# Kernel optimization log

Hardware: AMD Instinct MI355X
Metric: run time of the kernel (lower is better)

## Reference

```python
import jax, jax.numpy as jnp
import numpy as np

N, S, K, DIN, DOUT = 100000, 50000, 16, 256, 256


def setup_inputs() -> dict:
    key = jax.random.key(0)
    k1, k2, k3, k4 = jax.random.split(key, 4)
    word_vectors = jax.random.normal(k1, (N, DIN), dtype=jnp.float32)
    src_idx = jnp.arange(S, dtype=jnp.int64)  # unique source nodes
    neighs_idx = jax.random.randint(k2, (S, K), 0, N).astype(jnp.int64)
    src_mask = jax.random.uniform(k3, (S, K), dtype=jnp.float32)
    W = jax.random.normal(k4, (DOUT, DIN), dtype=jnp.float32) / np.sqrt(DIN)
    b = jnp.zeros((DOUT,), dtype=jnp.float32)
    return {"word_vectors": word_vectors, "src_idx": src_idx,
            "neighs_idx": neighs_idx, "src_mask": src_mask, "W": W, "b": b}


def reference(word_vectors, src_idx, neighs_idx, src_mask, W, b):
    # Linear projection: [N, DIN] @ [DIN, DOUT] + b -> [N, DOUT]
    supports = word_vectors @ W.T + b
    src_feats = supports[src_idx]          # [S, D]
    neigh_feats = supports[neighs_idx]     # [S, K, D]
    # masked neighbor aggregation ([S,1,K] x [S,K,D]) + residual
    outputs = jnp.einsum('sk,skd->sd', src_mask, neigh_feats) + src_feats
    # LeakyReLU(negative_slope=0.2)
    outputs = jnp.where(outputs >= 0, outputs, 0.2 * outputs)
    # scatter-add back into supports (src_idx unique -> matches torch in-place +=)
    supports = supports.at[src_idx].add(outputs)
    return supports
```

## Files before the change

kernel.cpp:

```cpp
#include <hip/hip_runtime.h>
#include <hip/hip_bf16.h>

#define DIN  256
#define DOUT 256
#define KNEI 16

typedef __attribute__((ext_vector_type(4))) float f32x4;
typedef __attribute__((ext_vector_type(8))) short bf16x8;
typedef __attribute__((ext_vector_type(4))) short bf16x4;

__device__ __forceinline__ short f2bf(float f) {
    unsigned int u;
    __builtin_memcpy(&u, &f, 4);
    unsigned int r = (u + 0x7fffu + ((u >> 16) & 1u)) >> 16;
    return (short)r;
}

__device__ __forceinline__ float bf2f(short s) {
    unsigned int u = ((unsigned int)(unsigned short)s) << 16;
    float f;
    __builtin_memcpy(&f, &u, 4);
    return f;
}

__global__ __launch_bounds__(256) void pack_w_kernel(
        const float* __restrict__ W, short* __restrict__ Wp) {
    int gid  = blockIdx.x * 256 + threadIdx.x;
    int lane = gid & 63;
    int frag = gid >> 6;
    int kb   = frag & 7;
    int cb   = frag >> 3;
    int col  = cb * 16 + (lane & 15);
    int k0   = kb * 32 + (lane >> 4) * 8;
    const float* src = W + (size_t)col * DIN + k0;
    bf16x8 v;
#pragma unroll
    for (int j = 0; j < 8; ++j) v[j] = f2bf(src[j]);
    *((bf16x8*)Wp + (size_t)frag * 64 + lane) = v;
}

__global__ __launch_bounds__(256) void gemm_kernel(
        const float* __restrict__ A, const short* __restrict__ Wp,
        const float* __restrict__ bias, float* __restrict__ out,
        short* __restrict__ out_bf, int M) {
    const int tid  = threadIdx.x;
    const int wid  = tid >> 6;
    const int lane = tid & 63;
    const int row0 = (blockIdx.x * 4 + wid) * 16;
    if (row0 >= M) return;

    const int r = row0 + (lane & 15);
    const int g = lane >> 4;

    const float* arow = A + (size_t)r * DIN + g * 8;
    f32x4 araw[16];
#pragma unroll
    for (int kb = 0; kb < 8; ++kb) {
        araw[2 * kb]     = *(const f32x4*)(arow + kb * 32);
        araw[2 * kb + 1] = *(const f32x4*)(arow + kb * 32 + 4);
    }
    bf16x8 afrag[8];
#pragma unroll
    for (int kb = 0; kb < 8; ++kb) {
#pragma unroll
        for (int j = 0; j < 4; ++j) {
            afrag[kb][j]     = f2bf(araw[2 * kb][j]);
            afrag[kb][4 + j] = f2bf(araw[2 * kb + 1][j]);
        }
    }

    f32x4 acc[16];
#pragma unroll
    for (int cb = 0; cb < 16; ++cb) acc[cb] = f32x4{0.f, 0.f, 0.f, 0.f};

    const bf16x8* wp = (const bf16x8*)Wp;
#pragma unroll
    for (int kb = 0; kb < 8; ++kb) {
#pragma unroll
        for (int cb = 0; cb < 16; ++cb) {
            bf16x8 w = wp[(size_t)(cb * 8 + kb) * 64 + lane];
            acc[cb] = __builtin_amdgcn_mfma_f32_16x16x32_bf16(
                w, afrag[kb], acc[cb], 0, 0, 0);
        }
    }

    float* orow = out    + (size_t)r * DOUT;
    short* brow = out_bf + (size_t)r * DOUT;
#pragma unroll
    for (int cb = 0; cb < 16; ++cb) {
        int c0 = cb * 16 + g * 4;
        f32x4 bv = *(const f32x4*)(bias + c0);
        f32x4 v  = acc[cb] + bv;
        __builtin_nontemporal_store(v, (f32x4*)(orow + c0));
        bf16x4 h;
#pragma unroll
        for (int j = 0; j < 4; ++j) h[j] = f2bf(v[j]);
        *(bf16x4*)(brow + c0) = h;
    }
}

__global__ __launch_bounds__(256) void aggregate_fused_kernel(
        const short* __restrict__ sup_bf, const int* __restrict__ src_idx,
        const int* __restrict__ neighs, const float* __restrict__ mask,
        float* __restrict__ out, int S) {
    int s = blockIdx.x * 4 + (threadIdx.x >> 6);
    if (s >= S) return;
    s = __builtin_amdgcn_readfirstlane(s);
    const int lane = threadIdx.x & 63;
    const int c4   = lane * 4;

    f32x4 acc = {0.f, 0.f, 0.f, 0.f};
#pragma unroll
    for (int k = 0; k < KNEI; ++k) {
        int   idx = neighs[(size_t)s * KNEI + k];
        float m   = mask[(size_t)s * KNEI + k];
        bf16x4 v = *(const bf16x4*)(sup_bf + (size_t)idx * DOUT + c4);
#pragma unroll
        for (int j = 0; j < 4; ++j) acc[j] += m * bf2f(v[j]);
    }

    int srow = src_idx[s];
    bf16x4 svh = *(const bf16x4*)(sup_bf + (size_t)srow * DOUT + c4);
    f32x4 res;
#pragma unroll
    for (int j = 0; j < 4; ++j) {
        float sv = bf2f(svh[j]);
        float o  = acc[j] + sv;
        o = (o >= 0.f) ? o : 0.2f * o;
        res[j] = sv + o;
    }
    __builtin_nontemporal_store(res, (f32x4*)(out + (size_t)srow * DOUT + c4));
}

__global__ __launch_bounds__(256) void aggregate_f32_kernel(
        const float* __restrict__ supports, const int* __restrict__ src_idx,
        const int* __restrict__ neighs, const float* __restrict__ mask,
        float* __restrict__ outrows, int S) {
    int s = blockIdx.x * 4 + (threadIdx.x >> 6);
    if (s >= S) return;
    s = __builtin_amdgcn_readfirstlane(s);
    const int lane = threadIdx.x & 63;
    const int c4   = lane * 4;
    f32x4 acc = {0.f, 0.f, 0.f, 0.f};
#pragma unroll
    for (int k = 0; k < KNEI; ++k) {
        int   idx = neighs[(size_t)s * KNEI + k];
        float m   = mask[(size_t)s * KNEI + k];
        f32x4 v = *(const f32x4*)(supports + (size_t)idx * DOUT + c4);
#pragma unroll
        for (int j = 0; j < 4; ++j) acc[j] += m * v[j];
    }
    int srow = src_idx[s];
    f32x4 sv = *(const f32x4*)(supports + (size_t)srow * DOUT + c4);
    f32x4 res;
#pragma unroll
    for (int j = 0; j < 4; ++j) {
        float o = acc[j] + sv[j];
        o = (o >= 0.f) ? o : 0.2f * o;
        res[j] = sv[j] + o;
    }
    *(f32x4*)(outrows + (size_t)s * DOUT + c4) = res;
}

__global__ __launch_bounds__(256) void scatter_kernel(
        const float* __restrict__ outrows, const int* __restrict__ src_idx,
        float* __restrict__ out, int S) {
    int gid = blockIdx.x * 256 + threadIdx.x;
    int s   = gid >> 6;
    if (s >= S) return;
    int lane = gid & 63;
    int row  = src_idx[s];
    *(f32x4*)(out + (size_t)row * DOUT + lane * 4) =
        *(const f32x4*)(outrows + (size_t)s * DOUT + lane * 4);
}

extern "C" void kernel_launch(void* const* d_in, const int* in_sizes, int n_in,
                              void* d_out, int out_size, void* d_ws, size_t ws_size,
                              hipStream_t stream) {
    (void)n_in; (void)out_size;
    const float* wv     = (const float*)d_in[0];
    const int*   src_i  = (const int*)d_in[1];
    const int*   neighs = (const int*)d_in[2];
    const float* mask   = (const float*)d_in[3];
    const float* W      = (const float*)d_in[4];
    const float* bias   = (const float*)d_in[5];
    float* out = (float*)d_out;

    const int N = in_sizes[0] / DIN;
    const int S = in_sizes[1];

    char*  ws      = (char*)d_ws;
    size_t sz_wp   = (size_t)DOUT * DIN * 2;
    size_t off_buf = (sz_wp + 1023) & ~(size_t)1023;
    short* Wp      = (short*)ws;
    short* sup_bf  = (short*)(ws + off_buf);
    float* outrows = (float*)(ws + off_buf);
    int fused = (ws_size >= off_buf + (size_t)N * DOUT * 2) ? 1 : 0;

    pack_w_kernel<<<32, 256, 0, stream>>>(W, Wp);

    int mwaves  = (N + 15) / 16;
    int mblocks = (mwaves + 3) / 4;
    gemm_kernel<<<mblocks, 256, 0, stream>>>(wv, Wp, bias, out, sup_bf, N);

    if (fused) {
        aggregate_fused_kernel<<<(S + 3) / 4, 256, 0, stream>>>(
            sup_bf, src_i, neighs, mask, out, S);
    } else {
        aggregate_f32_kernel<<<(S + 3) / 4, 256, 0, stream>>>(
            out, src_i, neighs, mask, outrows, S);
        scatter_kernel<<<((size_t)S * 64 + 255) / 256, 256, 0, stream>>>(
            outrows, src_i, out, S);
    }
}
```

Before: 144.6 us.

## Split GEMM columns across waves and skip f32 stores for source rows

The GEMM now gives each block 16 rows, with each of its four waves computing 64 output columns. Each wave preloads its W fragments into registers, so it issues 4 accumulators instead of 16. A byte mask of source rows is built first (zeroed inside the pack kernel, then set by a small kernel), and the GEMM skips writing f32 output for rows that the aggregate kernel will overwrite anyway. This saves about half of the f32 output write traffic, at the cost of an extra launch, a byte mask read per row, and four times as many GEMM blocks, each re-reading its A rows across four waves.

Result: slower. 161.9 us (+12.0%).

```diff
diff --git a/kernel.cpp b/kernel.cpp
--- a/kernel.cpp
+++ b/kernel.cpp
@@ -24,33 +24,47 @@
 }
 
 __global__ __launch_bounds__(256) void pack_w_kernel(
-        const float* __restrict__ W, short* __restrict__ Wp) {
-    int gid  = blockIdx.x * 256 + threadIdx.x;
-    int lane = gid & 63;
-    int frag = gid >> 6;
-    int kb   = frag & 7;
-    int cb   = frag >> 3;
-    int col  = cb * 16 + (lane & 15);
-    int k0   = kb * 32 + (lane >> 4) * 8;
-    const float* src = W + (size_t)col * DIN + k0;
-    bf16x8 v;
-#pragma unroll
-    for (int j = 0; j < 8; ++j) v[j] = f2bf(src[j]);
-    *((bf16x8*)Wp + (size_t)frag * 64 + lane) = v;
+        const float* __restrict__ W, short* __restrict__ Wp,
+        unsigned char* __restrict__ bm, int N) {
+    if (blockIdx.x < 32) {
+        int gid  = blockIdx.x * 256 + threadIdx.x;
+        int lane = gid & 63;
+        int frag = gid >> 6;
+        int kb   = frag & 7;
+        int cb   = frag >> 3;
+        int col  = cb * 16 + (lane & 15);
+        int k0   = kb * 32 + (lane >> 4) * 8;
+        const float* src = W + (size_t)col * DIN + k0;
+        bf16x8 v;
+#pragma unroll
+        for (int j = 0; j < 8; ++j) v[j] = f2bf(src[j]);
+        *((bf16x8*)Wp + (size_t)frag * 64 + lane) = v;
+    } else {
+        int i = (blockIdx.x - 32) * 256 + threadIdx.x;
+        if (i < N) bm[i] = 0;
+    }
+}
+
+__global__ __launch_bounds__(256) void set_bm_kernel(
+        const int* __restrict__ src_idx, unsigned char* __restrict__ bm, int S) {
+    int s = blockIdx.x * 256 + threadIdx.x;
+    if (s < S) bm[src_idx[s]] = 1;
 }
 
 __global__ __launch_bounds__(256) void gemm_kernel(
         const float* __restrict__ A, const short* __restrict__ Wp,
         const float* __restrict__ bias, float* __restrict__ out,
-        short* __restrict__ out_bf, int M) {
+        short* __restrict__ out_bf, const unsigned char* __restrict__ bm,
+        int M, int use_bm) {
     const int tid  = threadIdx.x;
     const int wid  = tid >> 6;
     const int lane = tid & 63;
-    const int row0 = (blockIdx.x * 4 + wid) * 16;
+    const int row0 = blockIdx.x * 16;
     if (row0 >= M) return;
 
-    const int r = row0 + (lane & 15);
-    const int g = lane >> 4;
+    const int rraw = row0 + (lane & 15);
+    const int r    = (rraw < M) ? rraw : (M - 1);
+    const int g    = lane >> 4;
 
     const float* arow = A + (size_t)r * DIN + g * 8;
     f32x4 araw[16];
@@ -59,6 +73,18 @@
         araw[2 * kb]     = *(const f32x4*)(arow + kb * 32);
         araw[2 * kb + 1] = *(const f32x4*)(arow + kb * 32 + 4);
     }
+
+    const bf16x8* wp = (const bf16x8*)Wp;
+    bf16x8 wfrag[8][4];
+#pragma unroll
+    for (int kb = 0; kb < 8; ++kb) {
+#pragma unroll
+        for (int j = 0; j < 4; ++j) {
+            int cb = wid * 4 + j;
+            wfrag[kb][j] = wp[(size_t)(cb * 8 + kb) * 64 + lane];
+        }
+    }
+
     bf16x8 afrag[8];
 #pragma unroll
     for (int kb = 0; kb < 8; ++kb) {
@@ -69,33 +95,32 @@
         }
     }
 
-    f32x4 acc[16];
-#pragma unroll
-    for (int cb = 0; cb < 16; ++cb) acc[cb] = f32x4{0.f, 0.f, 0.f, 0.f};
-
-    const bf16x8* wp = (const bf16x8*)Wp;
-#pragma unroll
-    for (int kb = 0; kb < 8; ++kb) {
-#pragma unroll
-        for (int cb = 0; cb < 16; ++cb) {
-            bf16x8 w = wp[(size_t)(cb * 8 + kb) * 64 + lane];
-            acc[cb] = __builtin_amdgcn_mfma_f32_16x16x32_bf16(
-                w, afrag[kb], acc[cb], 0, 0, 0);
-        }
-    }
-
+    f32x4 acc[4];
+#pragma unroll
+    for (int j = 0; j < 4; ++j) acc[j] = f32x4{0.f, 0.f, 0.f, 0.f};
+
+#pragma unroll
+    for (int kb = 0; kb < 8; ++kb) {
+#pragma unroll
+        for (int j = 0; j < 4; ++j)
+            acc[j] = __builtin_amdgcn_mfma_f32_16x16x32_bf16(
+                wfrag[kb][j], afrag[kb], acc[j], 0, 0, 0);
+    }
+
+    const bool wr = (rraw < M);
+    const bool store_f32 = wr && (!use_bm || bm[r] == 0);
     float* orow = out    + (size_t)r * DOUT;
     short* brow = out_bf + (size_t)r * DOUT;
 #pragma unroll
-    for (int cb = 0; cb < 16; ++cb) {
-        int c0 = cb * 16 + g * 4;
+    for (int j = 0; j < 4; ++j) {
+        int c0 = wid * 64 + j * 16 + g * 4;
         f32x4 bv = *(const f32x4*)(bias + c0);
-        f32x4 v  = acc[cb] + bv;
-        __builtin_nontemporal_store(v, (f32x4*)(orow + c0));
+        f32x4 v  = acc[j] + bv;
         bf16x4 h;
 #pragma unroll
-        for (int j = 0; j < 4; ++j) h[j] = f2bf(v[j]);
-        *(bf16x4*)(brow + c0) = h;
+        for (int q = 0; q < 4; ++q) h[q] = f2bf(v[q]);
+        if (wr) *(bf16x4*)(brow + c0) = h;
+        if (store_f32) *(f32x4*)(orow + c0) = v;
     }
 }
 
@@ -129,7 +154,7 @@
         o = (o >= 0.f) ? o : 0.2f * o;
         res[j] = sv + o;
     }
-    __builtin_nontemporal_store(res, (f32x4*)(out + (size_t)srow * DOUT + c4));
+    *(f32x4*)(out + (size_t)srow * DOUT + c4) = res;
 }
 
 __global__ __launch_bounds__(256) void aggregate_f32_kernel(
@@ -191,17 +216,22 @@
 
     char*  ws      = (char*)d_ws;
     size_t sz_wp   = (size_t)DOUT * DIN * 2;
-    size_t off_buf = (sz_wp + 1023) & ~(size_t)1023;
-    short* Wp      = (short*)ws;
-    short* sup_bf  = (short*)(ws + off_buf);
-    float* outrows = (float*)(ws + off_buf);
+    size_t off_bm  = (sz_wp + 1023) & ~(size_t)1023;
+    size_t off_buf = (off_bm + (size_t)N + 1023) & ~(size_t)1023;
+    short*         Wp      = (short*)ws;
+    unsigned char* bm      = (unsigned char*)(ws + off_bm);
+    short*         sup_bf  = (short*)(ws + off_buf);
+    float*         outrows = (float*)(ws + off_buf);
     int fused = (ws_size >= off_buf + (size_t)N * DOUT * 2) ? 1 : 0;
 
-    pack_w_kernel<<<32, 256, 0, stream>>>(W, Wp);
-
-    int mwaves  = (N + 15) / 16;
-    int mblocks = (mwaves + 3) / 4;
-    gemm_kernel<<<mblocks, 256, 0, stream>>>(wv, Wp, bias, out, sup_bf, N);
+    int zblocks = (N + 255) / 256;
+    pack_w_kernel<<<32 + zblocks, 256, 0, stream>>>(W, Wp, bm, N);
+    if (fused)
+        set_bm_kernel<<<(S + 255) / 256, 256, 0, stream>>>(src_i, bm, S);
+
+    int mblocks = (N + 15) / 16;
+    gemm_kernel<<<mblocks, 256, 0, stream>>>(
+        wv, Wp, bias, out, sup_bf, bm, N, fused);
 
     if (fused) {
         aggregate_fused_kernel<<<(S + 3) / 4, 256, 0, stream>>>(
```
